# Kernel tuning notes

Measured on AMD Instinct MI355X. Metric: run time of the kernel, lower is better.

## Reference

```python
import jax, jax.numpy as jnp
import numpy as np


def square_distance(src, dst):
    # src: [B,N,C], dst: [B,M,C] -> [B,N,M] squared euclidean distances
    # ||s||^2 + ||d||^2 - 2 s.d, same expansion as the torch module
    d = -2.0 * jnp.einsum('bnc,bmc->bnm', src, dst)
    d = d + jnp.sum(src * src, axis=-1)[:, :, None]
    d = d + jnp.sum(dst * dst, axis=-1)[:, None, :]
    return d


def setup_inputs() -> dict:
    key = jax.random.key(0)
    k1, k2 = jax.random.split(key)
    B, N, M, C = 32, 4096, 4096, 3
    x = jax.random.normal(k1, (B, N, C), dtype=jnp.float32)
    recon = jax.random.normal(k2, (B, M, C), dtype=jnp.float32)
    return {"x": x, "recon": recon}


def reference(x, recon):
    # Chamfer distance (get_loss). square_distance(recon, x) is the
    # transpose of square_distance(x, recon), so compute once.
    d = square_distance(x, recon)            # [B,N,M]
    cost_p2_p1 = jnp.min(d, axis=-1)         # min over recon for each x point
    cost_p1_p2 = jnp.min(d, axis=-2)         # min over x for each recon point
    loss = jnp.mean(cost_p1_p2) + jnp.mean(cost_p2_p1)
    return loss
```

## Files before the change

### kernel.cpp

```cpp
#include <hip/hip_runtime.h>
#include <float.h>
#include <stdint.h>


typedef short bf16x8 __attribute__((ext_vector_type(8)));
typedef float f32x16 __attribute__((ext_vector_type(16)));

#define BLK 256
#define ONE_BF 0x3F80u

__device__ __forceinline__ uint32_t bf16_rne(float f) {
    uint32_t u = __builtin_bit_cast(uint32_t, f);
    return (u + 0x7FFFu + ((u >> 16) & 1u)) >> 16;
}
__device__ __forceinline__ float bf16f(uint32_t h) {
    return __builtin_bit_cast(float, h << 16);
}

__global__ __launch_bounds__(BLK)
void prep_kernel(const float* __restrict__ x, const float* __restrict__ recon,
                 uint32_t* __restrict__ ws)
{
    int tid = blockIdx.x * BLK + threadIdx.x;
    int arr = tid >> 17;
    int p   = tid & 131071;
    const float* s = arr ? recon : x;
    float a = s[3 * p], b = s[3 * p + 1], c = s[3 * p + 2];
    uint32_t hx = bf16_rne(a), hy = bf16_rne(b), hz = bf16_rne(c);
    uint32_t lx = bf16_rne(a - bf16f(hx));
    uint32_t ly = bf16_rne(b - bf16f(hy));
    uint32_t lz = bf16_rne(c - bf16f(hz));
    float tt = a * a + b * b + c * c;
    uint32_t th = bf16_rne(tt);
    uint32_t tl = bf16_rne(tt - bf16f(th));
    uint4 H0 = make_uint4(hx | (hy << 16), hz | (hx << 16),
                          hy | (hz << 16), lx | (ly << 16));
    uint4 H1 = make_uint4(lz | (th << 16), tl | (lx << 16),
                          ly | (lz << 16), 0u);
    ((uint4*)ws)[tid]          = H0;
    ((uint4*)ws)[262144 + tid] = H1;
}

__global__ __launch_bounds__(BLK, 4)
void chamfer_mfma(const float* __restrict__ x, const float* __restrict__ recon,
                  const uint32_t* __restrict__ ws, float* __restrict__ out,
                  float scale)
{
    const int dir = blockIdx.y;
    const int qb  = blockIdx.x & 15;
    const int b   = blockIdx.x >> 4;
    const float* qsrc = dir ? recon : x;
    const int arrT = dir ? 0 : 1;

    const int tid  = threadIdx.x;
    const int wave = tid >> 6;
    const int lane = tid & 63;
    const int l31  = lane & 31;
    const int lh   = lane >> 5;

    bf16x8 A0, A1;
    {
        int n0 = qb * 256 + wave * 64 + l31;
        #pragma unroll
        for (int rb = 0; rb < 2; ++rb) {
            const float* qp = qsrc + ((size_t)b * 4096 + n0 + rb * 32) * 3;
            float cx = -2.f * qp[0], cy = -2.f * qp[1], cz = -2.f * qp[2];
            uint32_t hx = bf16_rne(cx), hy = bf16_rne(cy), hz = bf16_rne(cz);
            uint32_t lx = bf16_rne(cx - bf16f(hx));
            uint32_t ly = bf16_rne(cy - bf16f(hy));
            uint32_t lz = bf16_rne(cz - bf16f(hz));
            uint32_t w0, w1, w2, w3;
            if (lh == 0) {
                w0 = hx | (hy << 16); w1 = hz | (lx << 16);
                w2 = ly | (lz << 16); w3 = hx | (hy << 16);
            } else {
                w0 = hz | (ONE_BF << 16); w1 = ONE_BF | (lx << 16);
                w2 = ly | (lz << 16);     w3 = 0u;
            }
            union { uint4 u; bf16x8 v; } cvt;
            cvt.u = make_uint4(w0, w1, w2, w3);
            if (rb == 0) A0 = cvt.v; else A1 = cvt.v;
        }
    }

    f32x16 zc = {0,0,0,0,0,0,0,0,0,0,0,0,0,0,0,0};
    float rmn0[16], rmn1[16];
    #pragma unroll
    for (int j = 0; j < 16; ++j) { rmn0[j] = FLT_MAX; rmn1[j] = FLT_MAX; }

    const uint4* rec = (const uint4*)ws
        + (size_t)lh * 262144 + (size_t)arrT * 131072 + (size_t)b * 4096 + l31;

    #pragma unroll 2
    for (int it = 0; it < 128; ++it) {
        union { uint4 u; bf16x8 v; } Bf;
        Bf.u = rec[it * 32];
        f32x16 d0 = __builtin_amdgcn_mfma_f32_32x32x16_bf16(A0, Bf.v, zc, 0, 0, 0);
        f32x16 d1 = __builtin_amdgcn_mfma_f32_32x32x16_bf16(A1, Bf.v, zc, 0, 0, 0);
        #pragma unroll
        for (int j = 0; j < 16; ++j) {
            rmn0[j] = fminf(rmn0[j], d0[j]);
            rmn1[j] = fminf(rmn1[j], d1[j]);
        }
    }

    __shared__ float lmin[256][33];
    #pragma unroll
    for (int j = 0; j < 16; ++j) {
        int rl = (j & 3) + 8 * (j >> 2) + 4 * lh;
        lmin[wave * 64 + rl][l31]      = rmn0[j];
        lmin[wave * 64 + 32 + rl][l31] = rmn1[j];
    }
    __syncthreads();

    float m = lmin[tid][0];
    #pragma unroll
    for (int c = 1; c < 32; ++c) m = fminf(m, lmin[tid][c]);

    const float* qp = qsrc + ((size_t)b * 4096 + qb * 256 + tid) * 3;
    float v = m + qp[0] * qp[0] + qp[1] * qp[1] + qp[2] * qp[2];

    #pragma unroll
    for (int off = 32; off > 0; off >>= 1)
        v += __shfl_down(v, off, 64);
    __shared__ float red[4];
    if (lane == 0) red[wave] = v;
    __syncthreads();
    if (tid == 0)
        atomicAdd(out, (red[0] + red[1] + red[2] + red[3]) * scale);
}

extern "C" void kernel_launch(void* const* d_in, const int* in_sizes, int n_in,
                              void* d_out, int out_size, void* d_ws, size_t ws_size,
                              hipStream_t stream) {
    const float* x     = (const float*)d_in[0];
    const float* recon = (const float*)d_in[1];
    float* out = (float*)d_out;

    const float scale = 1.0f / (32.0f * 4096.0f);

    hipMemsetAsync(out, 0, sizeof(float), stream);

    prep_kernel<<<1024, BLK, 0, stream>>>(x, recon, (uint32_t*)d_ws);

    dim3 g(512, 2);
    chamfer_mfma<<<g, BLK, 0, stream>>>(x, recon, (const uint32_t*)d_ws,
                                        out, scale);
}
```

Measured before the change: 103.6 us.

## Fold memset into prep, swizzle block order, reorder MFMA loop with pairwise min

```diff
diff --git a/kernel.cpp b/kernel.cpp
--- a/kernel.cpp
+++ b/kernel.cpp
@@ -19,9 +19,10 @@
 
 __global__ __launch_bounds__(BLK)
 void prep_kernel(const float* __restrict__ x, const float* __restrict__ recon,
-                 uint32_t* __restrict__ ws)
+                 uint32_t* __restrict__ ws, float* __restrict__ out)
 {
     int tid = blockIdx.x * BLK + threadIdx.x;
+    if (tid == 0) out[0] = 0.0f;
     int arr = tid >> 17;
     int p   = tid & 131071;
     const float* s = arr ? recon : x;
@@ -41,14 +42,17 @@
     ((uint4*)ws)[262144 + tid] = H1;
 }
 
-__global__ __launch_bounds__(BLK, 4)
+__global__ __launch_bounds__(BLK, 3)
 void chamfer_mfma(const float* __restrict__ x, const float* __restrict__ recon,
                   const uint32_t* __restrict__ ws, float* __restrict__ out,
                   float scale)
 {
-    const int dir = blockIdx.y;
-    const int qb  = blockIdx.x & 15;
-    const int b   = blockIdx.x >> 4;
+    int idx = blockIdx.x;
+    int swz = (idx & 7) * 128 + (idx >> 3);
+    int dir = swz >> 9;
+    int b   = (swz >> 4) & 31;
+    int qb  = swz & 15;
+
     const float* qsrc = dir ? recon : x;
     const int arrT = dir ? 0 : 1;
 
@@ -88,20 +92,24 @@
     #pragma unroll
     for (int j = 0; j < 16; ++j) { rmn0[j] = FLT_MAX; rmn1[j] = FLT_MAX; }
 
-    const uint4* rec = (const uint4*)ws
+    const uint4* rp = (const uint4*)ws
         + (size_t)lh * 262144 + (size_t)arrT * 131072 + (size_t)b * 4096 + l31;
 
-    #pragma unroll 2
-    for (int it = 0; it < 128; ++it) {
-        union { uint4 u; bf16x8 v; } Bf;
-        Bf.u = rec[it * 32];
-        f32x16 d0 = __builtin_amdgcn_mfma_f32_32x32x16_bf16(A0, Bf.v, zc, 0, 0, 0);
-        f32x16 d1 = __builtin_amdgcn_mfma_f32_32x32x16_bf16(A1, Bf.v, zc, 0, 0, 0);
+    for (int it = 0; it < 64; ++it) {
+        union BU { uint4 u; bf16x8 v; } B0, B1;
+        B0.u = rp[0];
+        B1.u = rp[32];
+        rp += 64;
+        f32x16 d0 = __builtin_amdgcn_mfma_f32_32x32x16_bf16(A0, B0.v, zc, 0, 0, 0);
+        f32x16 d1 = __builtin_amdgcn_mfma_f32_32x32x16_bf16(A0, B1.v, zc, 0, 0, 0);
         #pragma unroll
-        for (int j = 0; j < 16; ++j) {
-            rmn0[j] = fminf(rmn0[j], d0[j]);
-            rmn1[j] = fminf(rmn1[j], d1[j]);
-        }
+        for (int j = 0; j < 16; ++j)
+            rmn0[j] = fminf(rmn0[j], fminf(d0[j], d1[j]));
+        f32x16 e0 = __builtin_amdgcn_mfma_f32_32x32x16_bf16(A1, B0.v, zc, 0, 0, 0);
+        f32x16 e1 = __builtin_amdgcn_mfma_f32_32x32x16_bf16(A1, B1.v, zc, 0, 0, 0);
+        #pragma unroll
+        for (int j = 0; j < 16; ++j)
+            rmn1[j] = fminf(rmn1[j], fminf(e0[j], e1[j]));
     }
 
     __shared__ float lmin[256][33];
@@ -139,11 +147,8 @@
 
     const float scale = 1.0f / (32.0f * 4096.0f);
 
-    hipMemsetAsync(out, 0, sizeof(float), stream);
+    prep_kernel<<<1024, BLK, 0, stream>>>(x, recon, (uint32_t*)d_ws, out);
 
-    prep_kernel<<<1024, BLK, 0, stream>>>(x, recon, (uint32_t*)d_ws);
-
-    dim3 g(512, 2);
-    chamfer_mfma<<<g, BLK, 0, stream>>>(x, recon, (const uint32_t*)d_ws,
-                                        out, scale);
+    chamfer_mfma<<<1024, BLK, 0, stream>>>(x, recon, (const uint32_t*)d_ws,
+                                           out, scale);
 }
```

Result: faster. 100.9 us (-2.6%).
